# Kernel optimization log

Hardware: AMD Instinct MI355X
Metric: run time of the kernel (lower is better)

## Reference

```python
import jax, jax.numpy as jnp
import numpy as np

N_P, N_D, N_S = 100000, 1000, 5000      # patients, drugs, diseases
C, H, L = 64, 4, 2                       # hidden, heads, layers
DH = C // H                              # head dim
IN_P, IN_D, IN_S = 64, 128, 64           # raw feature dims per node type
E_PD, E_DP, E_DS, E_PS = 300000, 300000, 100000, 100000
EPS = 1e-16


def setup_inputs() -> dict:
    key = jax.random.key(0)
    ks = jax.random.split(key, 20)

    def lin(k, fin, fout, prefix=()):
        return jax.random.normal(k, prefix + (fin, fout), jnp.float32) / np.sqrt(fin).astype(np.float32)

    def edges(k, e, n_src, n_dst):
        k1, k2 = jax.random.split(k)
        return jnp.stack([jax.random.randint(k1, (e,), 0, n_src),
                          jax.random.randint(k2, (e,), 0, n_dst)]).astype(jnp.int32)

    inp = {}
    inp['x_p'] = jax.random.normal(ks[0], (N_P, IN_P), jnp.float32)
    inp['x_d'] = jax.random.normal(ks[1], (N_D, IN_D), jnp.float32)
    inp['x_s'] = jax.random.normal(ks[2], (N_S, IN_S), jnp.float32)
    inp['Win_p'] = lin(ks[3], IN_P, C); inp['bin_p'] = jnp.zeros((C,), jnp.float32)
    inp['Win_d'] = lin(ks[4], IN_D, C); inp['bin_d'] = jnp.zeros((C,), jnp.float32)
    inp['Win_s'] = lin(ks[5], IN_S, C); inp['bin_s'] = jnp.zeros((C,), jnp.float32)
    inp['Wk'] = lin(ks[6], C, C, (L, 3)); inp['bk'] = jnp.zeros((L, 3, C), jnp.float32)
    inp['Wq'] = lin(ks[7], C, C, (L, 3)); inp['bq'] = jnp.zeros((L, 3, C), jnp.float32)
    inp['Wv'] = lin(ks[8], C, C, (L, 3)); inp['bv'] = jnp.zeros((L, 3, C), jnp.float32)
    inp['Wa'] = lin(ks[9], C, C, (L, 3)); inp['ba'] = jnp.zeros((L, 3, C), jnp.float32)
    inp['a_rel'] = jax.random.normal(ks[10], (L, 4, H, DH, DH), jnp.float32) / np.sqrt(DH).astype(np.float32)
    inp['m_rel'] = jax.random.normal(ks[11], (L, 4, H, DH, DH), jnp.float32) / np.sqrt(DH).astype(np.float32)
    inp['p_rel'] = jnp.ones((L, 4, H), jnp.float32)   # PyG inits rel prior to ones
    inp['skip'] = jnp.ones((L, 3), jnp.float32)       # PyG inits skip gate to ones
    inp['ei_pd'] = edges(ks[12], E_PD, N_P, N_D)  # patient -takes-> drug
    inp['ei_dp'] = edges(ks[13], E_DP, N_D, N_P)  # drug -taken_by-> patient
    inp['ei_ds'] = edges(ks[14], E_DS, N_D, N_S)  # drug -treats-> disease
    inp['ei_ps'] = edges(ks[15], E_PS, N_P, N_S)  # patient -has-> disease
    return inp


def _hgt(x_p, x_d, x_s, Win_p, bin_p, Win_d, bin_d, Win_s, bin_s,
         Wk, bk, Wq, bq, Wv, bv, Wa, ba, a_rel, m_rel, p_rel, skip,
         ei_pd, ei_dp, ei_ds, ei_ps):
    Ns = (N_P, N_D, N_S)
    # per-node-type input projection (lin_dict)
    xs = [x_p @ Win_p + bin_p, x_d @ Win_d + bin_d, x_s @ Win_s + bin_s]
    # (src_type, dst_type, edge_index) for each relation
    edge_defs = [(0, 1, ei_pd), (1, 0, ei_dp), (1, 2, ei_ds), (0, 2, ei_ps)]
    inv_sqrt_d = np.float32(1.0 / np.sqrt(DH))

    for l in range(L):  # HGTConv layers
        k_t = [(xs[t] @ Wk[l, t] + bk[l, t]).reshape(Ns[t], H, DH) for t in range(3)]
        q_t = [(xs[t] @ Wq[l, t] + bq[l, t]).reshape(Ns[t], H, DH) for t in range(3)]
        v_t = [(xs[t] @ Wv[l, t] + bv[l, t]).reshape(Ns[t], H, DH) for t in range(3)]
        out = [jnp.zeros((Ns[t], H, DH), xs[t].dtype) for t in range(3)]
        for r, (st, dt, ei) in enumerate(edge_defs):
            src, dst = ei[0], ei[1]
            # relation-specific head-wise transforms of K and V
            k_rel = jnp.einsum('nhd,hde->nhe', k_t[st], a_rel[l, r])
            v_rel = jnp.einsum('nhd,hde->nhe', v_t[st], m_rel[l, r])
            # attention logits per edge, per head: [E, H]
            alpha = (q_t[dt][dst] * k_rel[src]).sum(-1) * (p_rel[l, r] * inv_sqrt_d)
            # segment softmax over incoming edges of each dst node (per relation)
            mx = jax.ops.segment_max(alpha, dst, num_segments=Ns[dt])
            a = jnp.exp(alpha - jax.lax.stop_gradient(mx)[dst])
            den = jax.ops.segment_sum(a, dst, num_segments=Ns[dt])
            a = a / (den[dst] + EPS)
            # attention-weighted scatter-add of messages, grouped by 'sum'
            out[dt] = out[dt] + jax.ops.segment_sum(v_rel[src] * a[:, :, None], dst, num_segments=Ns[dt])
        new_xs = []
        for t in range(3):
            o = jax.nn.gelu(out[t].reshape(Ns[t], C), approximate=False) @ Wa[l, t] + ba[l, t]
            s = jax.nn.sigmoid(skip[l, t])  # learned skip gate (in == out channels)
            new_xs.append(s * o + (1.0 - s) * xs[t])
        xs = new_xs
    # concatenate node-type outputs along node axis: [N_P+N_D+N_S, C]
    return jnp.concatenate(xs, axis=0)


def reference(x_p, x_d, x_s, Win_p, bin_p, Win_d, bin_d, Win_s, bin_s,
              Wk, bk, Wq, bq, Wv, bv, Wa, ba, a_rel, m_rel, p_rel, skip,
              ei_pd, ei_dp, ei_ds, ei_ps):
    return _hgt(x_p, x_d, x_s, Win_p, bin_p, Win_d, bin_d, Win_s, bin_s,
                Wk, bk, Wq, bq, Wv, bv, Wa, ba, a_rel, m_rel, p_rel, skip,
                ei_pd, ei_dp, ei_ds, ei_ps)
```

## Files before the change

kernel.cpp:

```cpp
#include <hip/hip_runtime.h>
#include <cmath>

typedef unsigned short ush;
typedef __attribute__((ext_vector_type(8))) short short8;
typedef __attribute__((ext_vector_type(4))) float floatx4;

static constexpr int N_P = 100000, N_D = 1000, N_S = 5000, NT = N_P + N_D + N_S;
static constexpr int NC = 111000;
static constexpr int E_TOT = 800000;

static constexpr int NB0 = 128, NB2 = 64, NB3 = 64;
static constexpr int CH0 = (300000 + NB0 - 1) / NB0;
static constexpr int CH2 = (100000 + NB2 - 1) / NB2;
static constexpr int HB0_OFF = 0;
static constexpr int HB2_OFF = NB0 * 1000;
static constexpr int HB3_OFF = HB2_OFF + NB2 * 5000;
static constexpr int NCH0 = NB0 / 16, NCH2 = NB2 / 16;
static constexpr int CS0_OFF = 0;
static constexpr int CS2_OFF = NCH0 * 1000;
static constexpr int CS3_OFF = CS2_OFF + NCH2 * 5000;
static constexpr int NHIST = NB0 + NB2 + NB3;
static constexpr int NBLK_R1 = (300000 + 255) / 256;
static constexpr int NZB = (100000 + 255) / 256;

__device__ __forceinline__ float b2f(ush b) { return __uint_as_float(((unsigned)b) << 16); }
__device__ __forceinline__ ush f2b(float f) {
    unsigned u = __float_as_uint(f);
    return (ush)((u + 0x7FFFu + ((u >> 16) & 1u)) >> 16);
}

static constexpr size_t OFF_WINP = 0;
static constexpr size_t OFF_BINP = 4096;
static constexpr size_t OFF_WIND = 4160;
static constexpr size_t OFF_BIND = 12352;
static constexpr size_t OFF_WINS = 12416;
static constexpr size_t OFF_BINS = 16512;
static constexpr size_t OFF_WK = 16576;
static constexpr size_t OFF_BK = 41152;
static constexpr size_t OFF_WQ = 41536;
static constexpr size_t OFF_BQ = 66112;
static constexpr size_t OFF_WV = 66496;
static constexpr size_t OFF_BV = 91072;
static constexpr size_t OFF_WA = 91456;
static constexpr size_t OFF_BA = 116032;
static constexpr size_t OFF_AREL = 116416;
static constexpr size_t OFF_MREL = 124608;
static constexpr size_t OFF_PREL = 132800;
static constexpr size_t OFF_SKIP = 132832;
static constexpr size_t CW_TOTAL = 132838;
static constexpr int NCONVB = (int)((CW_TOTAL + 255) / 256);
static constexpr int NSCB = (NC + 1 + 255) / 256;

static constexpr size_t TWINP = 0;
static constexpr size_t TWIND = 4096;
static constexpr size_t TWINS = 12288;
static constexpr size_t TWQO = 16384;
static constexpr size_t TWAO = 40960;
static constexpr size_t TW_TOTAL = 65536;
static constexpr int NTWB = (int)(TW_TOTAL / 256);

struct ConvArgs {
    const void* src[18];
    long cum[19];
    int fl[18];
};

struct CsrB {
    const int* ei[3];
    const int* ei1;
};

__device__ __forceinline__ void hist_geom(int b, const CsrB& c, int& r, const int*& ei, int& E,
                                          int& ndst, int& e0, int& e1, int& hb) {
    if (b < NB0) {
        r = 0; ei = c.ei[0]; E = 300000; ndst = 1000;
        e0 = b * CH0; hb = HB0_OFF + b * 1000;
    } else if (b < NB0 + NB2) {
        r = 1; ei = c.ei[1]; E = 100000; ndst = 5000;
        e0 = (b - NB0) * CH2; hb = HB2_OFF + (b - NB0) * 5000;
    } else {
        r = 2; ei = c.ei[2]; E = 100000; ndst = 5000;
        e0 = (b - NB0 - NB2) * CH2; hb = HB3_OFF + (b - NB0 - NB2) * 5000;
    }
    e1 = min(E, e0 + ((r == 0) ? CH0 : CH2));
}

__device__ __forceinline__ bool cs_geom(int g, int& idx0, int& step) {
    if (g >= 48000) return false;
    if (g < 8000) {
        int c = g / 1000, d = g % 1000;
        idx0 = HB0_OFF + c * 16 * 1000 + d; step = 1000;
    } else if (g < 28000) {
        int gg = g - 8000, c = gg / 5000, d = gg % 5000;
        idx0 = HB2_OFF + c * 16 * 5000 + d; step = 5000;
    } else {
        int gg = g - 28000, c = gg / 5000, d = gg % 5000;
        idx0 = HB3_OFF + c * 16 * 5000 + d; step = 5000;
    }
    return true;
}

__global__ __launch_bounds__(256) void k1_kernel(ConvArgs a, ush* __restrict__ dst,
                                                 ush* __restrict__ tw,
                                                 int* __restrict__ cnt_r1, CsrB c,
                                                 int* __restrict__ HB) {
    const int b = blockIdx.x;
    if (b < NCONVB) {
        long g = (long)b * 256 + threadIdx.x;
        if (g >= (long)CW_TOTAL) return;
        int t = 0;
        while (g >= a.cum[t + 1]) t++;
        long i = g - a.cum[t];
        float v = a.fl[t] ? ((const float*)a.src[t])[i] : b2f(((const ush*)a.src[t])[i]);
        dst[g] = f2b(v);
    } else if (b < NCONVB + NZB) {
        int g = (b - NCONVB) * 256 + threadIdx.x;
        if (g < 100000) cnt_r1[g] = 0;
    } else if (b < NCONVB + NZB + NHIST) {
        __shared__ int h[5000];
        int r, E, ndst, e0, e1, hb;
        const int* ei;
        hist_geom(b - NCONVB - NZB, c, r, ei, E, ndst, e0, e1, hb);
        for (int d = threadIdx.x; d < ndst; d += 256) h[d] = 0;
        __syncthreads();
        for (int e = e0 + threadIdx.x; e < e1; e += 256) atomicAdd(&h[ei[E + e]], 1);
        __syncthreads();
        for (int d = threadIdx.x; d < ndst; d += 256) HB[hb + d] = h[d];
    } else {
        int g = (b - NCONVB - NZB - NHIST) * 256 + threadIdx.x;
        const void* src; int fl; long ibase; int e;
        if (g < 4096) { src = a.src[0]; fl = a.fl[0]; e = g; ibase = 0; }
        else if (g < 12288) { src = a.src[2]; fl = a.fl[2]; e = g - 4096; ibase = 0; }
        else if (g < 16384) { src = a.src[4]; fl = a.fl[4]; e = g - 12288; ibase = 0; }
        else if (g < 40960) { int ee = g - 16384; src = a.src[8]; fl = a.fl[8];
                              e = ee & 4095; ibase = (long)(ee >> 12) * 4096; }
        else { int ee = g - 40960; src = a.src[12]; fl = a.fl[12];
               e = ee & 4095; ibase = (long)(ee >> 12) * 4096; }
        int f = e >> 9, l = (e >> 3) & 63, j = e & 7;
        int s = f >> 2, cc = f & 3;
        long in = ibase + (long)(32 * s + ((l >> 4) << 3) + j) * 64 + 16 * cc + (l & 15);
        float v = fl ? ((const float*)src)[in] : b2f(((const ush*)src)[in]);
        tw[g] = f2b(v);
    }
}

template <int K>
__device__ __forceinline__ void stage_A(short* sA, const ush* __restrict__ X, int M, int row0) {
    for (int cid = threadIdx.x; cid < 64 * K / 8; cid += 256) {
        int r = cid / (K / 8), c0 = (cid % (K / 8)) * 8;
        int row = row0 + r;
        short8 v = {0, 0, 0, 0, 0, 0, 0, 0};
        if (row < M) v = *(const short8*)(const void*)(X + (size_t)row * K + c0);
        *(short8*)(&sA[r * (K + 8) + c0]) = v;
    }
}

template <int K>
__device__ __forceinline__ void stage_A_raw(short* sA, const void* __restrict__ X, int f,
                                            int M, int row0) {
    for (int cid = threadIdx.x; cid < 64 * K / 8; cid += 256) {
        int r = cid / (K / 8), c0 = (cid % (K / 8)) * 8;
        int row = row0 + r;
        short8 v = {0, 0, 0, 0, 0, 0, 0, 0};
        if (row < M) {
            if (f) {
                const floatx4* fp = (const floatx4*)((const float*)X + (size_t)row * K + c0);
                floatx4 f0 = fp[0], f1 = fp[1];
#pragma unroll
                for (int j = 0; j < 4; j++) v[j] = (short)f2b(f0[j]);
#pragma unroll
                for (int j = 0; j < 4; j++) v[4 + j] = (short)f2b(f1[j]);
            } else {
                v = *(const short8*)(const void*)((const ush*)X + (size_t)row * K + c0);
            }
        }
        *(short8*)(&sA[r * (K + 8) + c0]) = v;
    }
}

template <int K>
__device__ __forceinline__ void gemm_core64(const short* sA, short* sB,
                                            const ush* __restrict__ W, const ush* __restrict__ Bb,
                                            ush* __restrict__ Y, int M, int row0) {
    constexpr int NF = (K / 32) * 4;
    const int tid = threadIdx.x;
    for (int u = tid; u < NF * 64; u += 256)
        *(short8*)(&sB[u * 8]) = *(const short8*)(const void*)(W + (size_t)u * 8);
    __syncthreads();
    const int w = tid >> 6, l = tid & 63;
    floatx4 acc[4];
#pragma unroll
    for (int c = 0; c < 4; c++) {
        float bv = b2f(Bb[16 * c + (l & 15)]);
        acc[c] = (floatx4){bv, bv, bv, bv};
    }
#pragma unroll
    for (int s = 0; s < K / 32; s++) {
        short8 a = *(const short8*)(&sA[(16 * w + (l & 15)) * (K + 8) + 32 * s + ((l >> 4) << 3)]);
#pragma unroll
        for (int c = 0; c < 4; c++) {
            short8 b = *(const short8*)(&sB[(s * 4 + c) * 512 + l * 8]);
            acc[c] = __builtin_amdgcn_mfma_f32_16x16x32_bf16(a, b, acc[c], 0, 0, 0);
        }
    }
    __syncthreads();
#pragma unroll
    for (int c = 0; c < 4; c++)
#pragma unroll
        for (int r = 0; r < 4; r++)
            sB[(16 * w + ((l >> 4) << 2) + r) * 72 + 16 * c + (l & 15)] =
                (short)f2b(acc[c][r]);
    __syncthreads();
    for (int u = tid; u < 512; u += 256) {
        int r = u >> 3, c0 = (u & 7) * 8;
        int row = row0 + r;
        if (row < M)
            *(short8*)(Y + (size_t)row * 64 + c0) = *(const short8*)(&sB[r * 72 + c0]);
    }
}

template <int NP>
__device__ __forceinline__ void gemm_panels(short* sA, short* sB,
                                            const ush* __restrict__ Wq,
                                            const ush* __restrict__ Bq, ush* __restrict__ Yq,
                                            const ush* __restrict__ WeA,
                                            ush* __restrict__ YAk, ush* __restrict__ YAv,
                                            const ush* __restrict__ WeB,
                                            ush* __restrict__ YBk, ush* __restrict__ YBv,
                                            int M, int row0) {
    const int tid = threadIdx.x;
    const int w = tid >> 6, l = tid & 63;
    __syncthreads();
    short8 a0 = *(const short8*)(&sA[(16 * w + (l & 15)) * 72 + ((l >> 4) << 3)]);
    short8 a1 = *(const short8*)(&sA[(16 * w + (l & 15)) * 72 + 32 + ((l >> 4) << 3)]);
    ush* dst[5] = {Yq, YAk, YAv, YBk, YBv};
#pragma unroll
    for (int p = 0; p < NP; p++) {
        __syncthreads();
        const ush* base = (p == 0) ? Wq : ((p <= 2) ? WeA : WeB);
        const int nw = (p == 0) ? 4 : 8;
        const int moff = (p == 0 || p == 1 || p == 3) ? 0 : 4;
        for (int u = tid; u < 512; u += 256) {
            int f = u >> 6, k = u & 63;
            int s = f >> 2, c = f & 3;
            const ush* src = base + (size_t)(s * nw + moff + c) * 512;
            *(short8*)(&sB[f * 512 + k * 8]) = *(const short8*)(const void*)(src + k * 8);
        }
        __syncthreads();
        const ush* bias = (p == 0) ? Bq : ((p <= 2) ? WeA + 8192 : WeB + 8192);
        const int boff = (p == 0 || p == 1 || p == 3) ? 0 : 64;
        floatx4 acc[4];
#pragma unroll
        for (int c = 0; c < 4; c++) {
            float bv = b2f(bias[boff + 16 * c + (l & 15)]);
            acc[c] = (floatx4){bv, bv, bv, bv};
        }
#pragma unroll
        for (int c = 0; c < 4; c++) {
            short8 b0 = *(const short8*)(&sB[c * 512 + l * 8]);
            acc[c] = __builtin_amdgcn_mfma_f32_16x16x32_bf16(a0, b0, acc[c], 0, 0, 0);
            short8 b1 = *(const short8*)(&sB[(4 + c) * 512 + l * 8]);
            acc[c] = __builtin_amdgcn_mfma_f32_16x16x32_bf16(a1, b1, acc[c], 0, 0, 0);
        }
#pragma unroll
        for (int c = 0; c < 4; c++)
#pragma unroll
            for (int r = 0; r < 4; r++)
                sA[(16 * w + ((l >> 4) << 2) + r) * 72 + 16 * c + (l & 15)] =
                    (short)f2b(acc[c][r]);
        __syncthreads();
        ush* Y = dst[p];
        for (int u = tid; u < 512; u += 256) {
            int r = u >> 3, c0 = (u & 7) * 8;
            int row = row0 + r;
            if (row < M)
                *(short8*)(Y + (size_t)row * 64 + c0) = *(const short8*)(&sA[r * 72 + c0]);
        }
    }
}

struct K2Args {
    const void* raw[3];
    int f[3];
    const ush* W[3];
    const ush* Bb[3];
    ush* X;
    const int* HB;
    int* CS;
    int* cnt;
    const int* ei1;
};

__global__ __launch_bounds__(256) void k2_kernel(K2Args a) {
    extern __shared__ short smem[];
    const int b = blockIdx.x;
    if (b < 1658) {
        if (b < 1563) {
            short* sA = smem; short* sB = smem + 64 * 72;
            stage_A_raw<64>(sA, a.raw[0], a.f[0], N_P, b * 64);
            gemm_core64<64>(sA, sB, a.W[0], a.Bb[0], a.X, N_P, b * 64);
        } else if (b < 1579) {
            short* sA = smem; short* sB = smem + 64 * 136;
            stage_A_raw<128>(sA, a.raw[1], a.f[1], N_D, (b - 1563) * 64);
            gemm_core64<128>(sA, sB, a.W[1], a.Bb[1], a.X + (size_t)N_P * 64, N_D,
                             (b - 1563) * 64);
        } else {
            short* sA = smem; short* sB = smem + 64 * 72;
            stage_A_raw<64>(sA, a.raw[2], a.f[2], N_S, (b - 1579) * 64);
            gemm_core64<64>(sA, sB, a.W[2], a.Bb[2], a.X + (size_t)(N_P + N_D) * 64, N_S,
                            (b - 1579) * 64);
        }
    } else if (b < 1701) {
        int d = (b - 1658) * 256 + threadIdx.x;
        if (d >= 11000) return;
        int ld_, nch, base, step, cs0, csstep, roff;
        if (d < 1000) { ld_ = d; nch = NCH0; base = HB0_OFF + ld_; step = 1000;
                        cs0 = CS0_OFF + ld_; csstep = 1000; roff = 0; }
        else if (d < 6000) { ld_ = d - 1000; nch = NCH2; base = HB2_OFF + ld_; step = 5000;
                             cs0 = CS2_OFF + ld_; csstep = 5000; roff = 101000; }
        else { ld_ = d - 6000; nch = NCH2; base = HB3_OFF + ld_; step = 5000;
               cs0 = CS3_OFF + ld_; csstep = 5000; roff = 106000; }
        int run = 0;
        for (int cc = 0; cc < nch; cc++) {
            int s = 0;
#pragma unroll
            for (int bb = 0; bb < 16; bb++) s += a.HB[base + (cc * 16 + bb) * step];
            a.CS[cs0 + cc * csstep] = run;
            run += s;
        }
        a.cnt[roff + ld_] = run;
    } else {
        int g = (b - 1701) * 256 + threadIdx.x;
        if (g < 300000) atomicAdd(&a.cnt[1000 + a.ei1[300000 + g]], 1);
    }
}

__global__ __launch_bounds__(256) void k3_kernel(const int* __restrict__ cnt,
                                                 int* __restrict__ tmp,
                                                 int* __restrict__ part,
                                                 const ush* __restrict__ CW,
                                                 ush* __restrict__ weff) {
    const int b = blockIdx.x;
    if (b < 109) {
        __shared__ int ls[256];
        const int t = threadIdx.x;
        const int base = b * 1024 + t * 4;
        int v[4];
#pragma unroll
        for (int j = 0; j < 4; j++) v[j] = (base + j < NC) ? cnt[base + j] : 0;
        int tsum = v[0] + v[1] + v[2] + v[3];
        ls[t] = tsum;
        __syncthreads();
        for (int off = 1; off < 256; off <<= 1) {
            int y = (t >= off) ? ls[t - off] : 0;
            __syncthreads();
            ls[t] += y;
            __syncthreads();
        }
        int run = ls[t] - tsum;
#pragma unroll
        for (int j = 0; j < 4; j++) {
            if (base + j < NC) tmp[base + j] = run;
            run += v[j];
        }
        if (t == 255) part[b] = ls[255];
    } else {
        const int eb = b - 109;
        const int l = eb >> 2, r = eb & 3;
        const int st_of[4] = {0, 1, 1, 0};
        const int st = st_of[r];
        ush* out = weff + (size_t)eb * 8320;
        for (int idx = threadIdx.x; idx < 8320; idx += 256) {
            int k, n;
            if (idx < 8192) {
                int f = idx >> 9, ll = (idx >> 3) & 63, j = idx & 7;
                int s = f >> 3, c = f & 7;
                k = 32 * s + ((ll >> 4) << 3) + j;
                n = 16 * c + (ll & 15);
            } else { k = -1; n = idx - 8192; }
            int kv = n >= 64;
            int jj = n & 63, h = jj >> 4, e = jj & 15;
            const ush* W = CW + (kv ? OFF_WV : OFF_WK) + (size_t)(l * 3 + st) * 4096;
            const ush* B = CW + (kv ? OFF_BV : OFF_BK) + (size_t)(l * 3 + st) * 64;
            const ush* R = CW + (kv ? OFF_MREL : OFF_AREL) + (size_t)(l * 4 + r) * 1024;
            float acc = 0.f;
            if (k >= 0) {
#pragma unroll
                for (int d = 0; d < 16; d++)
                    acc += b2f(W[k * 64 + h * 16 + d]) * b2f(R[h * 256 + d * 16 + e]);
            } else {
#pragma unroll
                for (int d = 0; d < 16; d++)
                    acc += b2f(B[h * 16 + d]) * b2f(R[h * 256 + d * 16 + e]);
            }
            out[idx] = f2b(acc);
        }
    }
}

__global__ __launch_bounds__(256) void k4_kernel(const int* __restrict__ tmp,
                                                 const int* __restrict__ part,
                                                 int* __restrict__ rowptr,
                                                 int* __restrict__ HB,
                                                 const int* __restrict__ CS,
                                                 int* __restrict__ fillpos) {
    const int b = blockIdx.x;
    if (b < NSCB) {
        __shared__ int ls[256];
        const int t = threadIdx.x;
        ls[t] = (t < 109) ? part[t] : 0;
        __syncthreads();
        for (int off = 1; off < 256; off <<= 1) {
            int y = (t >= off) ? ls[t - off] : 0;
            __syncthreads();
            ls[t] += y;
            __syncthreads();
        }
        int i = b * 256 + t;
        if (i <= NC)
            rowptr[i] = (i == NC) ? ls[255] : tmp[i] + ((i >> 10) ? ls[(i >> 10) - 1] : 0);
    } else if (b < NSCB + 188) {
        int g = (b - NSCB) * 256 + threadIdx.x;
        int idx0, step;
        if (!cs_geom(g, idx0, step)) return;
        int run = CS[g];
#pragma unroll
        for (int bb = 0; bb < 16; bb++) {
            int t2 = HB[idx0 + bb * step];
            HB[idx0 + bb * step] = run;
            run += t2;
        }
    } else {
        int g = (b - NSCB - 188) * 256 + threadIdx.x;
        if (g < 100000) fillpos[g] = 0;
    }
}

struct QKVArgs {
    const ush* X;
    ush* Q;
    ush* KVk[4];
    ush* KVv[4];
    const ush* Wq[3];
    const ush* Bq[3];
    const ush* We[4];
};

__global__ __launch_bounds__(256) void qkv_kernel(QKVArgs a) {
    extern __shared__ short smem[];
    const int b = blockIdx.x;
    short* sA = smem;
    short* sB = smem + 64 * 72;
    if (b < 1563) {
        stage_A<64>(sA, a.X, N_P, b * 64);
        gemm_panels<5>(sA, sB, a.Wq[0], a.Bq[0], a.Q,
                       a.We[0], a.KVk[0], a.KVv[0],
                       a.We[3], a.KVk[3], a.KVv[3], N_P, b * 64);
    } else if (b < 1579) {
        int lb = b - 1563;
        stage_A<64>(sA, a.X + (size_t)N_P * 64, N_D, lb * 64);
        gemm_panels<5>(sA, sB, a.Wq[1], a.Bq[1], a.Q + (size_t)N_P * 64,
                       a.We[1], a.KVk[1], a.KVv[1],
                       a.We[2], a.KVk[2], a.KVv[2], N_D, lb * 64);
    } else {
        int lb = b - 1579;
        stage_A<64>(sA, a.X + (size_t)(N_P + N_D) * 64, N_S, lb * 64);
        gemm_panels<1>(sA, sB, a.Wq[2], a.Bq[2], a.Q + (size_t)(N_P + N_D) * 64,
                       nullptr, nullptr, nullptr, nullptr, nullptr, nullptr,
                       N_S, lb * 64);
    }
}

struct FillArgs {
    CsrB cb;
    const int* HB;
    const int* rowptr;
    int* fillpos;
    int* col;
};

__global__ __launch_bounds__(256) void fill_kernel(FillArgs a) {
    extern __shared__ short smem[];
    const int b = blockIdx.x;
    if (b < NHIST) {
        int* h = (int*)smem;
        int r, E, ndst, e0, e1, hb;
        const int* ei;
        hist_geom(b, a.cb, r, ei, E, ndst, e0, e1, hb);
        const int roff = (r == 0) ? 0 : (r == 1) ? 101000 : 106000;
        for (int d = threadIdx.x; d < ndst; d += 256) h[d] = a.rowptr[roff + d] + a.HB[hb + d];
        __syncthreads();
        for (int e = e0 + threadIdx.x; e < e1; e += 256) {
            int d = ei[E + e];
            int slot = atomicAdd(&h[d], 1);
            a.col[slot] = ei[e];
        }
    } else {
        int g = (b - NHIST) * 256 + threadIdx.x;
        if (g < 300000) {
            int gi = 1000 + a.cb.ei1[300000 + g];
            int slot = a.rowptr[gi] + atomicAdd(&a.fillpos[gi], 1);
            a.col[slot] = a.cb.ei1[g];
        }
    }
}

struct AggrArgs {
    const int* rowptr;
    const int* col;
    const ush* KVk[4];
    const ush* KVv[4];
    const ush* Q;
    const ush* prel;
    ush* OUT;
};

template <int LANES>
__device__ __forceinline__ void seg_attn(const AggrArgs& a, int rel, int g, int h, int lane,
                                         const float* qf, float* o) {
    const int s0 = a.rowptr[g], s1 = a.rowptr[g + 1];
    const ush* Kb = a.KVk[rel];
    const ush* Vb = a.KVv[rel];
// ... 90 lines not shown
        for (int i = 0; i < 16; i++) {
            float ao = __shfl_xor(acc[i], wd);
            acc[i] = acc[i] * e0 + ao * e1;
        }
        m = nm;
    }
    float inv = 1.f / (s + 1e-16f);
#pragma unroll
    for (int i = 0; i < 16; i++) o[i] += acc[i] * inv;
}

template <int LANES>
__device__ __forceinline__ void job_run(const AggrArgs& a, int wid, int nd, int rel, int roff,
                                        size_t xoff, int rel2, int roff2) {
    const int lane = wid % LANES;
    const int grp = wid / LANES;
    const int d = grp >> 2, h = grp & 3;
    if (d >= nd) return;
    const ush* qp = a.Q + xoff + (size_t)d * 64 + h * 16;
    short8 q0 = *(const short8*)(const void*)qp;
    short8 q1 = *(const short8*)(const void*)(qp + 8);
    float qf[16];
#pragma unroll
    for (int i = 0; i < 8; i++) { qf[i] = b2f((ush)q0[i]); qf[8 + i] = b2f((ush)q1[i]); }
    float o[16];
#pragma unroll
    for (int i = 0; i < 16; i++) o[i] = 0.f;
    seg_attn<LANES>(a, rel, roff + d, h, lane, qf, o);
    if (rel2 >= 0) seg_attn<LANES>(a, rel2, roff2 + d, h, lane, qf, o);
    if (lane == 0) {
        ush* op = a.OUT + xoff + (size_t)d * 64 + h * 16;
        short8 w0, w1;
#pragma unroll
        for (int i = 0; i < 8; i++) {
            float va = o[i];
            w0[i] = (short)f2b(0.5f * va * (1.0f + erff(va * 0.70710678118654752f)));
            float vb = o[8 + i];
            w1[i] = (short)f2b(0.5f * vb * (1.0f + erff(vb * 0.70710678118654752f)));
        }
        *(short8*)(op) = w0;
        *(short8*)(op + 8) = w1;
    }
}

__global__ __launch_bounds__(256) void aggr_kernel(AggrArgs a) {
    const int b = blockIdx.x, t = threadIdx.x;
    if (b < 250) {
        job_run<16>(a, b * 256 + t, N_D, 0, 0, (size_t)N_P * 64, -1, 0);
    } else if (b < 563) {
        job_run<4>(a, (b - 250) * 256 + t, N_S, 2, 101000, (size_t)(N_P + N_D) * 64, 3, 106000);
    } else {
        job_run<2>(a, (b - 563) * 256 + t, N_P, 1, 1000, 0, -1, 0);
    }
}

struct EpiArgs {
    const ush* O;
    ush* X;
    const ush* W[3];
    const ush* Bb[3];
    const ush* skipv;
    void* fout;
    int foutf;
    int last;
};

__global__ __launch_bounds__(256) void epi_kernel(EpiArgs a) {
    const int b = blockIdx.x;
    int t, lb, M;
    size_t noff;
    if (b < 1563) { t = 0; lb = b; M = N_P; noff = 0; }
    else if (b < 1579) { t = 1; lb = b - 1563; M = N_D; noff = (size_t)N_P; }
    else { t = 2; lb = b - 1579; M = N_S; noff = (size_t)(N_P + N_D); }
    const ush* O = a.O + noff * 64;
    ush* X = a.X + noff * 64;
    const ush* WF = a.W[t];
    __shared__ short sA[64 * 72];
    __shared__ short sB[8 * 512];
    const int tid = threadIdx.x;
    const int row0 = lb * 64;
    for (int cid = tid; cid < 512; cid += 256) {
        int r = cid >> 3, c0 = (cid & 7) * 8;
        int row = row0 + r;
        short8 sv = {0, 0, 0, 0, 0, 0, 0, 0};
        if (row < M) sv = *(const short8*)(const void*)(O + (size_t)row * 64 + c0);
        *(short8*)(&sA[r * 72 + c0]) = sv;
    }
    for (int u = tid; u < 512; u += 256)
        *(short8*)(&sB[u * 8]) = *(const short8*)(const void*)(WF + (size_t)u * 8);
    __syncthreads();
    const float sg = 1.f / (1.f + expf(-b2f(a.skipv[t])));
    const int w = tid >> 6, l = tid & 63;
    floatx4 acc[4];
#pragma unroll
    for (int c = 0; c < 4; c++) {
        float bv = b2f(a.Bb[t][16 * c + (l & 15)]);
        acc[c] = (floatx4){bv, bv, bv, bv};
    }
#pragma unroll
    for (int s = 0; s < 2; s++) {
        short8 av = *(const short8*)(&sA[(16 * w + (l & 15)) * 72 + 32 * s + ((l >> 4) << 3)]);
#pragma unroll
        for (int c = 0; c < 4; c++) {
            short8 bv = *(const short8*)(&sB[(s * 4 + c) * 512 + l * 8]);
            acc[c] = __builtin_amdgcn_mfma_f32_16x16x32_bf16(av, bv, acc[c], 0, 0, 0);
        }
// ... 40 lines not shown
                    } else {
                        short8 ov;
#pragma unroll
                        for (int j = 0; j < 8; j++) ov[j] = (short)f2b(vo[j]);
                        *(short8*)((ush*)a.fout + goff) = ov;
                    }
                }
            }
        }
    }
}

extern "C" void kernel_launch(void* const* d_in, const int* in_sizes, int n_in,
                              void* d_out, int out_size, void* d_ws, size_t ws_size,
                              hipStream_t stream) {
    char* w = (char*)d_ws;
    w += 64;
    ush* CW = (ush*)w;      w += ((CW_TOTAL * 2 + 63) / 64) * 64;
    ush* WEFFB = (ush*)w;   w += ((size_t)8 * 8320 * 2 + 63) / 64 * 64;
    ush* TW = (ush*)w;      w += (size_t)TW_TOTAL * 2;
    ush* X = (ush*)w;       w += (size_t)NT * 64 * 2;
    ush* Q = (ush*)w;       w += (size_t)NT * 64 * 2;
    ush* KV0 = (ush*)w;     w += (size_t)N_P * 128 * 2;
    ush* KV1 = (ush*)w;     w += (size_t)N_D * 128 * 2;
    ush* KV2 = (ush*)w;     w += (size_t)N_D * 128 * 2;
    ush* KV3 = (ush*)w;     w += (size_t)N_P * 128 * 2;
    ush* OUT = (ush*)w;     w += (size_t)NT * 64 * 4;
    int* CNT = (int*)w;     w += (size_t)NC * 4;
    int* TMP = (int*)w;     w += (size_t)NC * 4;
    int* PART = (int*)w;    w += 512;
    int* ROWPTR = (int*)w;  w += (size_t)(NC + 1) * 4;
    int* COL = (int*)w;     w += (size_t)E_TOT * 4;
    int* HB = (int*)OUT;
    int* CS = (int*)OUT + 800000;

    static const long sz[18] = {4096, 64, 8192, 64, 4096, 64, 24576, 384, 24576, 384,
                                24576, 384, 24576, 384, 8192, 8192, 32, 6};
    ConvArgs ca;
    long cum = 0;
    for (int t = 0; t < 18; t++) {
        ca.src[t] = d_in[3 + t];
        ca.cum[t] = cum;
        ca.fl[t] = (in_sizes[3 + t] != (int)(sz[t] * 2)) ? 1 : 0;
        cum += sz[t];
    }
    ca.cum[18] = cum;

    CsrB cb;
    cb.ei[0] = (const int*)d_in[21];
    cb.ei[1] = (const int*)d_in[23];
    cb.ei[2] = (const int*)d_in[24];
    cb.ei1 = (const int*)d_in[22];

    k1_kernel<<<NCONVB + NZB + NHIST + NTWB, 256, 0, stream>>>(ca, CW, TW, CNT + 1000, cb, HB);

    K2Args k2;
    k2.raw[0] = d_in[0]; k2.f[0] = (in_sizes[0] != N_P * 64 * 2) ? 1 : 0;
    k2.raw[1] = d_in[1]; k2.f[1] = (in_sizes[1] != N_D * 128 * 2) ? 1 : 0;
    k2.raw[2] = d_in[2]; k2.f[2] = (in_sizes[2] != N_S * 64 * 2) ? 1 : 0;
    k2.W[0] = TW + TWINP; k2.Bb[0] = CW + OFF_BINP;
    k2.W[1] = TW + TWIND; k2.Bb[1] = CW + OFF_BIND;
    k2.W[2] = TW + TWINS; k2.Bb[2] = CW + OFF_BINS;
    k2.X = X;
    k2.HB = HB; k2.CS = CS; k2.cnt = CNT; k2.ei1 = cb.ei1;
    k2_kernel<<<1701 + NBLK_R1, 256, 33792, stream>>>(k2);

    k3_kernel<<<109 + 8, 256, 0, stream>>>(CNT, TMP, PART, CW, WEFFB);

    k4_kernel<<<NSCB + 188 + NZB, 256, 0, stream>>>(TMP, PART, ROWPTR, HB, CS, CNT + 1000);

    ush* KVr[4] = {KV0, KV1, KV2, KV3};
    const size_t nsr[4] = {(size_t)N_P, (size_t)N_D, (size_t)N_D, (size_t)N_P};
    const int foutf = (out_size != NT * 64 * 2) ? 1 : 0;

    for (int l = 0; l < 2; l++) {
        QKVArgs qk;
        qk.X = X;
        qk.Q = Q;
        for (int r = 0; r < 4; r++) {
            qk.KVk[r] = KVr[r];
            qk.KVv[r] = KVr[r] + nsr[r] * 64;
            qk.We[r] = WEFFB + (size_t)(l * 4 + r) * 8320;
        }
        for (int t = 0; t < 3; t++) {
            qk.Wq[t] = TW + TWQO + (size_t)(l * 3 + t) * 4096;
            qk.Bq[t] = CW + OFF_BQ + (l * 3 + t) * 64;
        }
        qkv_kernel<<<1658, 256, 17408, stream>>>(qk);

        if (l == 0) {
            FillArgs fa;
            fa.cb = cb;
            fa.HB = HB;
            fa.rowptr = ROWPTR;
            fa.fillpos = CNT;
            fa.col = COL;
            fill_kernel<<<NHIST + NBLK_R1, 256, 20000, stream>>>(fa);
        }

        AggrArgs aa;
        aa.rowptr = ROWPTR;
        aa.col = COL;
        for (int r = 0; r < 4; r++) {
            aa.KVk[r] = KVr[r];
            aa.KVv[r] = KVr[r] + nsr[r] * 64;
        }
        aa.Q = Q;
        aa.prel = CW + OFF_PREL + l * 16;
        aa.OUT = OUT;
        aggr_kernel<<<3688, 256, 0, stream>>>(aa);

        EpiArgs ea;
        ea.O = OUT;
        ea.X = X;
        for (int t = 0; t < 3; t++) {
            ea.W[t] = TW + TWAO + (size_t)(l * 3 + t) * 4096;
            ea.Bb[t] = CW + OFF_BA + (l * 3 + t) * 64;
        }
        ea.skipv = CW + OFF_SKIP + l * 3;
        ea.fout = d_out;
        ea.foutf = foutf;
        ea.last = (l == 1) ? 1 : 0;
        epi_kernel<<<1658, 256, 0, stream>>>(ea);
    }
}
```

Measured before the change: 350.2 us.

## Fuse input projection and epilogue with QKV panels, move Weff build into k1

```diff
diff --git a/kernel.cpp b/kernel.cpp
--- a/kernel.cpp
+++ b/kernel.cpp
@@ -27,6 +27,9 @@
 __device__ __forceinline__ ush f2b(float f) {
     unsigned u = __float_as_uint(f);
     return (ush)((u + 0x7FFFu + ((u >> 16) & 1u)) >> 16);
+}
+__device__ __forceinline__ float ldr(const void* p, int fl, long i) {
+    return fl ? b2f(f2b(((const float*)p)[i])) : b2f(((const ush*)p)[i]);
 }
 
 static constexpr size_t OFF_WINP = 0;
@@ -103,7 +106,8 @@
 __global__ __launch_bounds__(256) void k1_kernel(ConvArgs a, ush* __restrict__ dst,
                                                  ush* __restrict__ tw,
                                                  int* __restrict__ cnt_r1, CsrB c,
-                                                 int* __restrict__ HB) {
+                                                 int* __restrict__ HB,
+                                                 ush* __restrict__ weff) {
     const int b = blockIdx.x;
     if (b < NCONVB) {
         long g = (long)b * 256 + threadIdx.x;
@@ -126,7 +130,7 @@
         for (int e = e0 + threadIdx.x; e < e1; e += 256) atomicAdd(&h[ei[E + e]], 1);
         __syncthreads();
         for (int d = threadIdx.x; d < ndst; d += 256) HB[hb + d] = h[d];
-    } else {
+    } else if (b < NCONVB + NZB + NHIST + NTWB) {
         int g = (b - NCONVB - NZB - NHIST) * 256 + threadIdx.x;
         const void* src; int fl; long ibase; int e;
         if (g < 4096) { src = a.src[0]; fl = a.fl[0]; e = g; ibase = 0; }
@@ -141,17 +145,45 @@
         long in = ibase + (long)(32 * s + ((l >> 4) << 3) + j) * 64 + 16 * cc + (l & 15);
         float v = fl ? ((const float*)src)[in] : b2f(((const ush*)src)[in]);
         tw[g] = f2b(v);
-    }
-}
-
-template <int K>
-__device__ __forceinline__ void stage_A(short* sA, const ush* __restrict__ X, int M, int row0) {
-    for (int cid = threadIdx.x; cid < 64 * K / 8; cid += 256) {
-        int r = cid / (K / 8), c0 = (cid % (K / 8)) * 8;
-        int row = row0 + r;
-        short8 v = {0, 0, 0, 0, 0, 0, 0, 0};
-        if (row < M) v = *(const short8*)(const void*)(X + (size_t)row * K + c0);
-        *(short8*)(&sA[r * (K + 8) + c0]) = v;
+    } else {
+        const int eb = b - NCONVB - NZB - NHIST - NTWB;
+        const int l = eb >> 2, r = eb & 3;
+        const int st_of[4] = {0, 1, 1, 0};
+        const int st = st_of[r];
+        ush* out = weff + (size_t)eb * 8320;
+        for (int idx = threadIdx.x; idx < 8320; idx += 256) {
+            int k, n;
+            if (idx < 8192) {
+                int f = idx >> 9, ll = (idx >> 3) & 63, j = idx & 7;
+                int s = f >> 3, cc = f & 7;
+                k = 32 * s + ((ll >> 4) << 3) + j;
+                n = 16 * cc + (ll & 15);
+            } else { k = -1; n = idx - 8192; }
+            int kv = n >= 64;
+            int jj = n & 63, h = jj >> 4, e = jj & 15;
+            const void* Wp = kv ? a.src[10] : a.src[6];
+            const int flW = kv ? a.fl[10] : a.fl[6];
+            const void* Bp = kv ? a.src[11] : a.src[7];
+            const int flB = kv ? a.fl[11] : a.fl[7];
+            const void* Rp = kv ? a.src[15] : a.src[14];
+            const int flR = kv ? a.fl[15] : a.fl[14];
+            const long wb = (long)(l * 3 + st) * 4096;
+            const long bb = (long)(l * 3 + st) * 64;
+            const long rb = (long)(l * 4 + r) * 1024;
+            float acc = 0.f;
+            if (k >= 0) {
+#pragma unroll
+                for (int d = 0; d < 16; d++)
+                    acc += ldr(Wp, flW, wb + k * 64 + h * 16 + d) *
+                           ldr(Rp, flR, rb + h * 256 + d * 16 + e);
+            } else {
+#pragma unroll
+                for (int d = 0; d < 16; d++)
+                    acc += ldr(Bp, flB, bb + h * 16 + d) *
+                           ldr(Rp, flR, rb + h * 256 + d * 16 + e);
+            }
+            out[idx] = f2b(acc);
+        }
     }
 }
 
@@ -178,44 +210,40 @@
     }
 }
 
-template <int K>
-__device__ __forceinline__ void gemm_core64(const short* sA, short* sB,
-                                            const ush* __restrict__ W, const ush* __restrict__ Bb,
-                                            ush* __restrict__ Y, int M, int row0) {
-    constexpr int NF = (K / 32) * 4;
+__device__ __forceinline__ void stage_A_half(short* sA, const void* __restrict__ X, int f,
+                                             int M, int row0, int half) {
+    for (int cid = threadIdx.x; cid < 512; cid += 256) {
+        int r = cid >> 3, c0 = (cid & 7) * 8;
+        int row = row0 + r;
+        short8 v = {0, 0, 0, 0, 0, 0, 0, 0};
+        if (row < M) {
+            long off = (long)row * 128 + half * 64 + c0;
+            if (f) {
+                const floatx4* fp = (const floatx4*)((const float*)X + off);
+                floatx4 f0 = fp[0], f1 = fp[1];
+#pragma unroll
+                for (int j = 0; j < 4; j++) v[j] = (short)f2b(f0[j]);
+#pragma unroll
+                for (int j = 0; j < 4; j++) v[4 + j] = (short)f2b(f1[j]);
+            } else {
+                v = *(const short8*)(const void*)((const ush*)X + off);
+            }
+        }
+        *(short8*)(&sA[r * 72 + c0]) = v;
+    }
+}
+
+__device__ __forceinline__ void mfma64_acc(const short* sA, const short* sB, floatx4* acc) {
     const int tid = threadIdx.x;
-    for (int u = tid; u < NF * 64; u += 256)
-        *(short8*)(&sB[u * 8]) = *(const short8*)(const void*)(W + (size_t)u * 8);
-    __syncthreads();
     const int w = tid >> 6, l = tid & 63;
-    floatx4 acc[4];
-#pragma unroll
-    for (int c = 0; c < 4; c++) {
-        float bv = b2f(Bb[16 * c + (l & 15)]);
-        acc[c] = (floatx4){bv, bv, bv, bv};
-    }
-#pragma unroll
-    for (int s = 0; s < K / 32; s++) {
-        short8 a = *(const short8*)(&sA[(16 * w + (l & 15)) * (K + 8) + 32 * s + ((l >> 4) << 3)]);
+#pragma unroll
+    for (int s = 0; s < 2; s++) {
+        short8 av = *(const short8*)(&sA[(16 * w + (l & 15)) * 72 + 32 * s + ((l >> 4) << 3)]);
 #pragma unroll
         for (int c = 0; c < 4; c++) {
-            short8 b = *(const short8*)(&sB[(s * 4 + c) * 512 + l * 8]);
-            acc[c] = __builtin_amdgcn_mfma_f32_16x16x32_bf16(a, b, acc[c], 0, 0, 0);
-        }
-    }
-    __syncthreads();
-#pragma unroll
-    for (int c = 0; c < 4; c++)
-#pragma unroll
-        for (int r = 0; r < 4; r++)
-            sB[(16 * w + ((l >> 4) << 2) + r) * 72 + 16 * c + (l & 15)] =
-                (short)f2b(acc[c][r]);
-    __syncthreads();
-    for (int u = tid; u < 512; u += 256) {
-        int r = u >> 3, c0 = (u & 7) * 8;
-        int row = row0 + r;
-        if (row < M)
-            *(short8*)(Y + (size_t)row * 64 + c0) = *(const short8*)(&sB[r * 72 + c0]);
+            short8 bv = *(const short8*)(&sB[(s * 4 + c) * 512 + l * 8]);
+            acc[c] = __builtin_amdgcn_mfma_f32_16x16x32_bf16(av, bv, acc[c], 0, 0, 0);
+        }
     }
 }
 
@@ -279,37 +307,94 @@
     }
 }
 
-struct K2Args {
+__device__ __forceinline__ void run_panels(int t, short* sA, short* sB,
+                                           const ush* const* Wq, const ush* const* Bq,
+                                           const ush* const* We, ush* Q,
+                                           ush* const* KVk, ush* const* KVv,
+                                           int M, int row0) {
+    if (t == 0)
+        gemm_panels<5>(sA, sB, Wq[0], Bq[0], Q, We[0], KVk[0], KVv[0],
+                       We[3], KVk[3], KVv[3], M, row0);
+    else if (t == 1)
+        gemm_panels<5>(sA, sB, Wq[1], Bq[1], Q + (size_t)N_P * 64, We[1], KVk[1], KVv[1],
+                       We[2], KVk[2], KVv[2], M, row0);
+    else
+        gemm_panels<1>(sA, sB, Wq[2], Bq[2], Q + (size_t)(N_P + N_D) * 64,
+                       nullptr, nullptr, nullptr, nullptr, nullptr, nullptr, M, row0);
+}
+
+struct K2FArgs {
     const void* raw[3];
     int f[3];
-    const ush* W[3];
-    const ush* Bb[3];
+    const ush* Wi[3];
+    const ush* Bi[3];
     ush* X;
+    const ush* Wq[3];
+    const ush* Bq[3];
+    const ush* We[4];
+    ush* Q;
+    ush* KVk[4];
+    ush* KVv[4];
     const int* HB;
     int* CS;
     int* cnt;
     const int* ei1;
 };
 
-__global__ __launch_bounds__(256) void k2_kernel(K2Args a) {
+__global__ __launch_bounds__(256) void k2f_kernel(K2FArgs a) {
     extern __shared__ short smem[];
     const int b = blockIdx.x;
     if (b < 1658) {
-        if (b < 1563) {
-            short* sA = smem; short* sB = smem + 64 * 72;
-            stage_A_raw<64>(sA, a.raw[0], a.f[0], N_P, b * 64);
-            gemm_core64<64>(sA, sB, a.W[0], a.Bb[0], a.X, N_P, b * 64);
-        } else if (b < 1579) {
-            short* sA = smem; short* sB = smem + 64 * 136;
-            stage_A_raw<128>(sA, a.raw[1], a.f[1], N_D, (b - 1563) * 64);
-            gemm_core64<128>(sA, sB, a.W[1], a.Bb[1], a.X + (size_t)N_P * 64, N_D,
-                             (b - 1563) * 64);
+        short* sA = smem;
+        short* sB = smem + 64 * 72;
+        const int tid = threadIdx.x;
+        const int w = tid >> 6, l = tid & 63;
+        int t, lb, M;
+        if (b < 1563) { t = 0; lb = b; M = N_P; }
+        else if (b < 1579) { t = 1; lb = b - 1563; M = N_D; }
+        else { t = 2; lb = b - 1579; M = N_S; }
+        const size_t noff = (t == 0) ? 0 : (t == 1) ? (size_t)N_P : (size_t)(N_P + N_D);
+        const int row0 = lb * 64;
+        floatx4 acc[4];
+#pragma unroll
+        for (int c = 0; c < 4; c++) {
+            float bv = b2f(a.Bi[t][16 * c + (l & 15)]);
+            acc[c] = (floatx4){bv, bv, bv, bv};
+        }
+        if (t != 1) {
+            stage_A_raw<64>(sA, a.raw[t], a.f[t], M, row0);
+            for (int u = tid; u < 512; u += 256)
+                *(short8*)(&sB[u * 8]) = *(const short8*)(const void*)(a.Wi[t] + (size_t)u * 8);
+            __syncthreads();
+            mfma64_acc(sA, sB, acc);
         } else {
-            short* sA = smem; short* sB = smem + 64 * 72;
-            stage_A_raw<64>(sA, a.raw[2], a.f[2], N_S, (b - 1579) * 64);
-            gemm_core64<64>(sA, sB, a.W[2], a.Bb[2], a.X + (size_t)(N_P + N_D) * 64, N_S,
-                            (b - 1579) * 64);
-        }
+#pragma unroll
+            for (int hh = 0; hh < 2; hh++) {
+                if (hh) __syncthreads();
+                stage_A_half(sA, a.raw[1], a.f[1], M, row0, hh);
+                for (int u = tid; u < 512; u += 256)
+                    *(short8*)(&sB[u * 8]) =
+                        *(const short8*)(const void*)(a.Wi[1] + (size_t)hh * 4096 + (size_t)u * 8);
+                __syncthreads();
+                mfma64_acc(sA, sB, acc);
+            }
+        }
+        __syncthreads();
+#pragma unroll
+        for (int c = 0; c < 4; c++)
+#pragma unroll
+            for (int r = 0; r < 4; r++)
+                sA[(16 * w + ((l >> 4) << 2) + r) * 72 + 16 * c + (l & 15)] =
+                    (short)f2b(acc[c][r]);
+        __syncthreads();
+        ush* Xb = a.X + noff * 64;
+        for (int u = tid; u < 512; u += 256) {
+            int r = u >> 3, c0 = (u & 7) * 8;
+            int row = row0 + r;
+            if (row < M)
+                *(short8*)(Xb + (size_t)row * 64 + c0) = *(const short8*)(&sA[r * 72 + c0]);
+        }
+        run_panels(t, sA, sB, a.Wq, a.Bq, a.We, a.Q, a.KVk, a.KVv, M, row0);
     } else if (b < 1701) {
         int d = (b - 1658) * 256 + threadIdx.x;
         if (d >= 11000) return;
@@ -337,65 +422,30 @@
 
 __global__ __launch_bounds__(256) void k3_kernel(const int* __restrict__ cnt,
                                                  int* __restrict__ tmp,
-                                                 int* __restrict__ part,
-                                                 const ush* __restrict__ CW,
-                                                 ush* __restrict__ weff) {
+                                                 int* __restrict__ part) {
     const int b = blockIdx.x;
-    if (b < 109) {
-        __shared__ int ls[256];
-        const int t = threadIdx.x;
-        const int base = b * 1024 + t * 4;
-        int v[4];
-#pragma unroll
-        for (int j = 0; j < 4; j++) v[j] = (base + j < NC) ? cnt[base + j] : 0;
-        int tsum = v[0] + v[1] + v[2] + v[3];
-        ls[t] = tsum;
-        __syncthreads();
-        for (int off = 1; off < 256; off <<= 1) {
-            int y = (t >= off) ? ls[t - off] : 0;
-            __syncthreads();
-            ls[t] += y;
-            __syncthreads();
-        }
-        int run = ls[t] - tsum;
-#pragma unroll
-        for (int j = 0; j < 4; j++) {
-            if (base + j < NC) tmp[base + j] = run;
-            run += v[j];
-        }
-        if (t == 255) part[b] = ls[255];
-    } else {
-        const int eb = b - 109;
-        const int l = eb >> 2, r = eb & 3;
-        const int st_of[4] = {0, 1, 1, 0};
-        const int st = st_of[r];
-        ush* out = weff + (size_t)eb * 8320;
-        for (int idx = threadIdx.x; idx < 8320; idx += 256) {
-            int k, n;
-            if (idx < 8192) {
-                int f = idx >> 9, ll = (idx >> 3) & 63, j = idx & 7;
-                int s = f >> 3, c = f & 7;
-                k = 32 * s + ((ll >> 4) << 3) + j;
-                n = 16 * c + (ll & 15);
-            } else { k = -1; n = idx - 8192; }
-            int kv = n >= 64;
-            int jj = n & 63, h = jj >> 4, e = jj & 15;
-            const ush* W = CW + (kv ? OFF_WV : OFF_WK) + (size_t)(l * 3 + st) * 4096;
-            const ush* B = CW + (kv ? OFF_BV : OFF_BK) + (size_t)(l * 3 + st) * 64;
-            const ush* R = CW + (kv ? OFF_MREL : OFF_AREL) + (size_t)(l * 4 + r) * 1024;
-            float acc = 0.f;
-            if (k >= 0) {
-#pragma unroll
-                for (int d = 0; d < 16; d++)
-                    acc += b2f(W[k * 64 + h * 16 + d]) * b2f(R[h * 256 + d * 16 + e]);
-            } else {
-#pragma unroll
-                for (int d = 0; d < 16; d++)
-                    acc += b2f(B[h * 16 + d]) * b2f(R[h * 256 + d * 16 + e]);
-            }
-            out[idx] = f2b(acc);
-        }
-    }
+    __shared__ int ls[256];
+    const int t = threadIdx.x;
+    const int base = b * 1024 + t * 4;
+    int v[4];
+#pragma unroll
+    for (int j = 0; j < 4; j++) v[j] = (base + j < NC) ? cnt[base + j] : 0;
+    int tsum = v[0] + v[1] + v[2] + v[3];
+    ls[t] = tsum;
+    __syncthreads();
+    for (int off = 1; off < 256; off <<= 1) {
+        int y = (t >= off) ? ls[t - off] : 0;
+        __syncthreads();
+        ls[t] += y;
+        __syncthreads();
+    }
+    int run = ls[t] - tsum;
+#pragma unroll
+    for (int j = 0; j < 4; j++) {
+        if (base + j < NC) tmp[base + j] = run;
+        run += v[j];
+    }
+    if (t == 255) part[b] = ls[255];
 }
 
 __global__ __launch_bounds__(256) void k4_kernel(const int* __restrict__ tmp,
@@ -433,41 +483,6 @@
     } else {
         int g = (b - NSCB - 188) * 256 + threadIdx.x;
         if (g < 100000) fillpos[g] = 0;
-    }
-}
-
-struct QKVArgs {
-    const ush* X;
-    ush* Q;
-    ush* KVk[4];
-    ush* KVv[4];
-    const ush* Wq[3];
-    const ush* Bq[3];
-    const ush* We[4];
-};
-
-__global__ __launch_bounds__(256) void qkv_kernel(QKVArgs a) {
-    extern __shared__ short smem[];
-    const int b = blockIdx.x;
-    short* sA = smem;
-    short* sB = smem + 64 * 72;
-    if (b < 1563) {
-        stage_A<64>(sA, a.X, N_P, b * 64);
-        gemm_panels<5>(sA, sB, a.Wq[0], a.Bq[0], a.Q,
-                       a.We[0], a.KVk[0], a.KVv[0],
-                       a.We[3], a.KVk[3], a.KVv[3], N_P, b * 64);
-    } else if (b < 1579) {
-        int lb = b - 1563;
-        stage_A<64>(sA, a.X + (size_t)N_P * 64, N_D, lb * 64);
-        gemm_panels<5>(sA, sB, a.Wq[1], a.Bq[1], a.Q + (size_t)N_P * 64,
-                       a.We[1], a.KVk[1], a.KVv[1],
-                       a.We[2], a.KVk[2], a.KVv[2], N_D, lb * 64);
-    } else {
-        int lb = b - 1579;
-        stage_A<64>(sA, a.X + (size_t)(N_P + N_D) * 64, N_S, lb * 64);
-        gemm_panels<1>(sA, sB, a.Wq[2], a.Bq[2], a.Q + (size_t)(N_P + N_D) * 64,
-                       nullptr, nullptr, nullptr, nullptr, nullptr, nullptr,
-                       N_S, lb * 64);
     }
 }
 
@@ -664,6 +679,81 @@
     } else {
         job_run<2>(a, (b - 563) * 256 + t, N_P, 1, 1000, 0, -1, 0);
     }
+}
+
+struct Epi0Args {
+    const ush* O;
+    ush* X;
+    const ush* Wa[3];
+    const ush* Ba[3];
+    const ush* skipv;
+    const ush* Wq[3];
+    const ush* Bq[3];
+    const ush* We[4];
+    ush* Q;
+    ush* KVk[4];
+    ush* KVv[4];
+};
+
+__global__ __launch_bounds__(256) void epi0_kernel(Epi0Args a) {
+    extern __shared__ short smem[];
+    short* sA = smem;
+    short* sB = smem + 64 * 72;
+    const int b = blockIdx.x;
+    int t, lb, M;
+    size_t noff;
+    if (b < 1563) { t = 0; lb = b; M = N_P; noff = 0; }
+    else if (b < 1579) { t = 1; lb = b - 1563; M = N_D; noff = (size_t)N_P; }
+    else { t = 2; lb = b - 1579; M = N_S; noff = (size_t)(N_P + N_D); }
+    const ush* O = a.O + noff * 64;
+    ush* X = a.X + noff * 64;
+    const int tid = threadIdx.x;
+    const int w = tid >> 6, l = tid & 63;
+    const int row0 = lb * 64;
+    for (int u = tid; u < 512; u += 256) {
+        int r = u >> 3, c0 = (u & 7) * 8;
+        int row = row0 + r;
+        short8 sv = {0, 0, 0, 0, 0, 0, 0, 0};
+        if (row < M) sv = *(const short8*)(const void*)(O + (size_t)row * 64 + c0);
+        *(short8*)(&sA[r * 72 + c0]) = sv;
+    }
+    for (int u = tid; u < 512; u += 256)
+        *(short8*)(&sB[u * 8]) = *(const short8*)(const void*)(a.Wa[t] + (size_t)u * 8);
+    __syncthreads();
+    floatx4 acc[4];
+#pragma unroll
+    for (int c = 0; c < 4; c++) {
+        float bv = b2f(a.Ba[t][16 * c + (l & 15)]);
+        acc[c] = (floatx4){bv, bv, bv, bv};
+    }
+    mfma64_acc(sA, sB, acc);
+    __syncthreads();
+    for (int u = tid; u < 512; u += 256) {
+        int r = u >> 3, c0 = (u & 7) * 8;
+        int row = row0 + r;
+        if (row < M)
+            *(short8*)(&sA[r * 72 + c0]) =
+                *(const short8*)(const void*)(X + (size_t)row * 64 + c0);
+    }
+    __syncthreads();
+    const float sg = 1.f / (1.f + expf(-b2f(a.skipv[t])));
+#pragma unroll
+    for (int c = 0; c < 4; c++)
+#pragma unroll
+        for (int r = 0; r < 4; r++) {
+            int rr = 16 * w + ((l >> 4) << 2) + r;
+            int cc = 16 * c + (l & 15);
+            float val = sg * acc[c][r] + (1.f - sg) * b2f((ush)sA[rr * 72 + cc]);
+            sA[rr * 72 + cc] = (short)f2b(val);
+        }
+    __syncthreads();
+    for (int u = tid; u < 512; u += 256) {
+        int r = u >> 3, c0 = (u & 7) * 8;
+        int row = row0 + r;
+        if (row < M)
+            *(short8*)(X + (size_t)row * 64 + c0) = *(const short8*)(&sA[r * 72 + c0]);
+    }
+    run_panels(t, sA, sB, a.Wq, a.Bq, a.We, a.Q, a.KVk, a.KVv, M, row0);
 }
 
 struct EpiArgs {
@@ -810,75 +900,89 @@
     cb.ei[2] = (const int*)d_in[24];
     cb.ei1 = (const int*)d_in[22];
 
-    k1_kernel<<<NCONVB + NZB + NHIST + NTWB, 256, 0, stream>>>(ca, CW, TW, CNT + 1000, cb, HB);
-
-    K2Args k2;
+    k1_kernel<<<NCONVB + NZB + NHIST + NTWB + 8, 256, 0, stream>>>(ca, CW, TW, CNT + 1000,
+                                                                   cb, HB, WEFFB);
+
+    ush* KVr[4] = {KV0, KV1, KV2, KV3};
+    const size_t nsr[4] = {(size_t)N_P, (size_t)N_D, (size_t)N_D, (size_t)N_P};
+    const int foutf = (out_size != NT * 64 * 2) ? 1 : 0;
+
+    K2FArgs k2;
     k2.raw[0] = d_in[0]; k2.f[0] = (in_sizes[0] != N_P * 64 * 2) ? 1 : 0;
     k2.raw[1] = d_in[1]; k2.f[1] = (in_sizes[1] != N_D * 128 * 2) ? 1 : 0;
     k2.raw[2] = d_in[2]; k2.f[2] = (in_sizes[2] != N_S * 64 * 2) ? 1 : 0;
-    k2.W[0] = TW + TWINP; k2.Bb[0] = CW + OFF_BINP;
-    k2.W[1] = TW + TWIND; k2.Bb[1] = CW + OFF_BIND;
-    k2.W[2] = TW + TWINS; k2.Bb[2] = CW + OFF_BINS;
+    k2.Wi[0] = TW + TWINP; k2.Bi[0] = CW + OFF_BINP;
+    k2.Wi[1] = TW + TWIND; k2.Bi[1] = CW + OFF_BIND;
+    k2.Wi[2] = TW + TWINS; k2.Bi[2] = CW + OFF_BINS;
     k2.X = X;
+    for (int t = 0; t < 3; t++) {
+        k2.Wq[t] = TW + TWQO + (size_t)(0 * 3 + t) * 4096;
+        k2.Bq[t] = CW + OFF_BQ + (0 * 3 + t) * 64;
+    }
+    for (int r = 0; r < 4; r++) {
+        k2.We[r] = WEFFB + (size_t)(0 * 4 + r) * 8320;
+        k2.KVk[r] = KVr[r];
+        k2.KVv[r] = KVr[r] + nsr[r] * 64;
+    }
+    k2.Q = Q;
     k2.HB = HB; k2.CS = CS; k2.cnt = CNT; k2.ei1 = cb.ei1;
-    k2_kernel<<<1701 + NBLK_R1, 256, 33792, stream>>>(k2);
-
-    k3_kernel<<<109 + 8, 256, 0, stream>>>(CNT, TMP, PART, CW, WEFFB);
+    k2f_kernel<<<1701 + NBLK_R1, 256, 17408, stream>>>(k2);
+
+    k3_kernel<<<109, 256, 0, stream>>>(CNT, TMP, PART);
 
     k4_kernel<<<NSCB + 188 + NZB, 256, 0, stream>>>(TMP, PART, ROWPTR, HB, CS, CNT + 1000);
 
-    ush* KVr[4] = {KV0, KV1, KV2, KV3};
-    const size_t nsr[4] = {(size_t)N_P, (size_t)N_D, (size_t)N_D, (size_t)N_P};
-    const int foutf = (out_size != NT * 64 * 2) ? 1 : 0;
-
-    for (int l = 0; l < 2; l++) {
-        QKVArgs qk;
-        qk.X = X;
-        qk.Q = Q;
-        for (int r = 0; r < 4; r++) {
-            qk.KVk[r] = KVr[r];
-            qk.KVv[r] = KVr[r] + nsr[r] * 64;
-            qk.We[r] = WEFFB + (size_t)(l * 4 + r) * 8320;
-        }
-        for (int t = 0; t < 3; t++) {
-            qk.Wq[t] = TW + TWQO + (size_t)(l * 3 + t) * 4096;
-            qk.Bq[t] = CW + OFF_BQ + (l * 3 + t) * 64;
-        }
-        qkv_kernel<<<1658, 256, 17408, stream>>>(qk);
-
-        if (l == 0) {
-            FillArgs fa;
-            fa.cb = cb;
-            fa.HB = HB;
-            fa.rowptr = ROWPTR;
-            fa.fillpos = CNT;
-            fa.col = COL;
-            fill_kernel<<<NHIST + NBLK_R1, 256, 20000, stream>>>(fa);
-        }
-
-        AggrArgs aa;
-        aa.rowptr = ROWPTR;
-        aa.col = COL;
-        for (int r = 0; r < 4; r++) {
-            aa.KVk[r] = KVr[r];
-            aa.KVv[r] = KVr[r] + nsr[r] * 64;
-        }
-        aa.Q = Q;
-        aa.prel = CW + OFF_PREL + l * 16;
-        aa.OUT = OUT;
-        aggr_kernel<<<3688, 256, 0, stream>>>(aa);
-
-        EpiArgs ea;
-        ea.O = OUT;
-        ea.X = X;
-        for (int t = 0; t < 3; t++) {
-            ea.W[t] = TW + TWAO + (size_t)(l * 3 + t) * 4096;
-            ea.Bb[t] = CW + OFF_BA + (l * 3 + t) * 64;
-        }
-        ea.skipv = CW + OFF_SKIP + l * 3;
-        ea.fout = d_out;
-        ea.foutf = foutf;
-        ea.last = (l == 1) ? 1 : 0;
-        epi_kernel<<<1658, 256, 0, stream>>>(ea);
-    }
-}
+    FillArgs fa;
+    fa.cb = cb;
+    fa.HB = HB;
+    fa.rowptr = ROWPTR;
+    fa.fillpos = CNT;
+    fa.col = COL;
+    fill_kernel<<<NHIST + NBLK_R1, 256, 20000, stream>>>(fa);
+
+    AggrArgs aa;
+    aa.rowptr = ROWPTR;
+    aa.col = COL;
+    for (int r = 0; r < 4; r++) {
+        aa.KVk[r] = KVr[r];
+        aa.KVv[r] = KVr[r] + nsr[r] * 64;
+    }
+    aa.Q = Q;
+    aa.prel = CW + OFF_PREL + 0 * 16;
+    aa.OUT = OUT;
+    aggr_kernel<<<3688, 256, 0, stream>>>(aa);
+
+    Epi0Args e0;
+    e0.O = OUT;
+    e0.X = X;
+    for (int t = 0; t < 3; t++) {
+        e0.Wa[t] = TW + TWAO + (size_t)(0 * 3 + t) * 4096;
+        e0.Ba[t] = CW + OFF_BA + (0 * 3 + t) * 64;
+        e0.Wq[t] = TW + TWQO + (size_t)(1 * 3 + t) * 4096;
+        e0.Bq[t] = CW + OFF_BQ + (1 * 3 + t) * 64;
+    }
+    e0.skipv = CW + OFF_SKIP + 0 * 3;
+    for (int r = 0; r < 4; r++) {
+        e0.We[r] = WEFFB + (size_t)(1 * 4 + r) * 8320;
+        e0.KVk[r] = KVr[r];
+        e0.KVv[r] = KVr[r] + nsr[r] * 64;
+    }
+    e0.Q = Q;
+    epi0_kernel<<<1658, 256, 17408, stream>>>(e0);
+
+    aa.prel = CW + OFF_PREL + 1 * 16;
+    aggr_kernel<<<3688, 256, 0, stream>>>(aa);
+
+    EpiArgs ea;
+    ea.O = OUT;
+    ea.X = X;
+    for (int t = 0; t < 3; t++) {
+        ea.W[t] = TW + TWAO + (size_t)(1 * 3 + t) * 4096;
+        ea.Bb[t] = CW + OFF_BA + (1 * 3 + t) * 64;
+    }
+    ea.skipv = CW + OFF_SKIP + 1 * 3;
+    ea.fout = d_out;
+    ea.foutf = foutf;
+    ea.last = 1;
+    epi_kernel<<<1658, 256, 0, stream>>>(ea);
+}
```

After: 427.4 us. 1.22x slower.
